# Kernel optimization log

Hardware: AMD Instinct MI355X
Metric: run time of the kernel (lower is better)

## Reference

```python
import jax, jax.numpy as jnp
import numpy as np

EPS = 1e-9
LAM_SEL, LAM_ID, LAM_RATE, LAM_KL, LAM_ENT, LAM_SMOOTH = 1.0, 10.0, 5.0, 0.1, 0.05, 0.5


def setup_inputs() -> dict:
    T, BS, V, K, RIDS = 48, 256, 4096, 32, 1024
    key = jax.random.key(0)
    ks = jax.random.split(key, 10)
    selector_logits = jax.random.normal(ks[0], (BS, 2, K), dtype=jnp.float32)
    selector_probs = jax.nn.softmax(jax.random.normal(ks[1], (BS, 2, K)), axis=-1)
    sel_idx = jax.random.randint(ks[2], (BS, 2), 0, K)
    selector_onehot = jax.nn.one_hot(sel_idx, K, dtype=jnp.float32)
    out_ids = jax.nn.softmax(jax.random.normal(ks[3], (T, BS, V)), axis=-1)
    out_rates = jax.random.uniform(ks[4], (T, BS, 1), dtype=jnp.float32)
    lab_idx = jax.random.randint(ks[5], (T + 2, BS), 0, V)
    trg_labels = jax.nn.one_hot(lab_idx, V, dtype=jnp.float32)
    trg_rates = jax.random.uniform(ks[6], (T + 2, BS, 1), dtype=jnp.float32)
    trg_lengths = jax.random.randint(ks[7], (BS,), 4, T + 2).astype(jnp.int32)
    candi_ids = jax.random.randint(ks[8], (BS, 2, K), 0, RIDS).astype(jnp.int32)
    routes = jax.random.randint(ks[9], (BS, V), 0, RIDS).astype(jnp.int32)
    return {
        'selector_logits': selector_logits, 'selector_probs': selector_probs,
        'selector_onehot': selector_onehot, 'out_ids': out_ids, 'out_rates': out_rates,
        'trg_labels': trg_labels, 'trg_rates': trg_rates, 'trg_lengths': trg_lengths,
        'candi_ids': candi_ids, 'routes': routes,
    }


def _align(lab, T_pred):
    T_lab = lab.shape[0]
    if T_lab >= T_pred + 2:
        return lab[1:-1]
    elif T_lab == T_pred:
        return lab
    else:
        pad = T_pred - T_lab
        return jnp.concatenate([lab, jnp.repeat(lab[-1:], pad, axis=0)], axis=0)


def _loss(selector_logits, selector_probs, selector_onehot, out_ids, out_rates,
          trg_labels, trg_rates, trg_lengths, candi_ids, routes):
    bs, _, K = selector_probs.shape
    # --- selector NLL (use_bce_logits=False path) ---
    sel_mask = (selector_onehot.sum(-1) > 0.5).astype(jnp.float32)      # [bs,2]
    sel_p_true = jnp.maximum((selector_probs * selector_onehot).sum(-1), EPS)
    loss_sel = (-jnp.log(sel_p_true) * sel_mask).sum() / jnp.maximum(sel_mask.sum(), 1.0)

    # --- id NLL over aligned target labels ---
    T_pred = out_ids.shape[0]
    tla = _align(trg_labels, T_pred)                                    # [T,bs,V]
    tra = _align(trg_rates, T_pred)                                     # [T,bs,1]
    step_mask = (tla.sum(-1) > 0.5).astype(jnp.float32)                 # [T,bs]
    p_true = jnp.maximum((out_ids * tla).sum(-1), EPS)
    loss_id = (-jnp.log(p_true) * step_mask).sum() * LAM_ID / jnp.maximum(step_mask.sum(), 1.0)

    # --- rate L1 ---
    denom_rate = jnp.maximum(1, (trg_lengths - 2).sum()).astype(jnp.float32)
    loss_rate = jnp.abs(out_rates - tra).sum() * LAM_RATE / denom_rate

    # --- KL over per-batch candidate unions (vectorized dedup via first-occurrence) ---
    U2 = 2 * K
    ids = candi_ids.reshape(bs, U2)                                     # [bs,2K]
    probs_flat = selector_probs.reshape(bs, U2)                         # [bs,2K]
    eq = ids[:, :, None] == ids[:, None, :]                             # [bs,2K,2K]
    rep = jnp.argmax(eq, axis=-1)                                       # first occurrence idx
    slots = jnp.arange(U2)
    valid = (rep == slots[None, :]).astype(jnp.float32)                 # [bs,2K] union slots
    Ucnt = valid.sum(-1)                                                # [bs]
    # Pm: scatter-add selector probs onto union slots (duplicates summed)
    rep_oh = (rep[:, :, None] == slots[None, None, :]).astype(jnp.float32)  # [bs,2K,2K]
    Pm = jnp.einsum('biu,bi->bu', rep_oh, probs_flat)                   # [bs,2K]
    Pm = Pm / jnp.maximum(Pm.sum(-1, keepdims=True), EPS)
    # Pb: project route mass onto union ids
    dist_r = out_ids.sum(0)                                             # [bs,V]
    match = (routes[:, :, None] == ids[:, None, :]).astype(jnp.float32)  # [bs,V,2K]
    agg = jnp.einsum('bvu,bv->bu', match, dist_r) * valid               # [bs,2K]
    s = agg.sum(-1, keepdims=True)                                      # [bs,1]
    uniform = valid / jnp.maximum(Ucnt, 1.0)[:, None]
    Pb = jnp.where(s > 0, agg / jnp.maximum(s, EPS), uniform)
    Pb_c = jnp.maximum(Pb, EPS)
    kl_b = (Pb_c * (jnp.log(Pb_c) - jnp.log(jnp.maximum(Pm, EPS))) * valid).sum(-1)
    loss_kl = LAM_KL * (kl_b.sum() / max(1, bs))

    # --- entropy of selector probs ---
    p = jnp.maximum(selector_probs, EPS)                                # [bs,2,K]
    ent_b = 0.5 * (-(p * jnp.log(p)).sum(-1)).sum(-1)                   # [bs]
    loss_entropy = LAM_ENT * (ent_b.sum() / max(1, bs))

    # --- rate smoothness ---
    r = out_rates[..., 0]                                               # [T,bs]
    dr = jnp.abs(r[1:] - r[:-1])                                        # [T-1,bs]
    eff = jnp.maximum(trg_lengths - 3, 0)                               # [bs]
    smask = (jnp.arange(T_pred - 1)[:, None] < eff[None, :]).astype(jnp.float32)
    loss_smooth = LAM_SMOOTH * (dr * smask).sum()

    return LAM_SEL * loss_sel + loss_id + loss_rate + loss_kl + loss_entropy + loss_smooth


def reference(selector_logits, selector_probs, selector_onehot, out_ids, out_rates,
              trg_labels, trg_rates, trg_lengths, candi_ids, routes):
    return _loss(selector_logits, selector_probs, selector_onehot, out_ids, out_rates,
                 trg_labels, trg_rates, trg_lengths, candi_ids, routes)
```

## Files before the change

kernel.cpp:

```cpp
#include <hip/hip_runtime.h>
#include <math.h>

#define EPSF 1e-9f

typedef float v4f __attribute__((ext_vector_type(4)));


__global__ __launch_bounds__(256) void e2e3_prep(
    const float* __restrict__ selector_probs,
    const int*   __restrict__ candi_ids,
    const int*   __restrict__ routes,
    float* __restrict__ pmlog_g,
    float* __restrict__ valid_g,
    signed char* __restrict__ slot_map,
    float* __restrict__ agg_g,
    float* __restrict__ acc)
{
    const int b   = blockIdx.x;
    const int tid = threadIdx.x;

    __shared__ int   ids_s[64];
    __shared__ int   table[1024];
    __shared__ int   rep_s[64];

    if (tid < 64) agg_g[b * 64 + tid] = 0.f;
    if (b == 0 && tid < 4) acc[tid] = 0.f;

    for (int i = tid; i < 1024; i += 256) table[i] = 64;
    if (tid < 64) ids_s[tid] = candi_ids[b * 64 + tid];
    __syncthreads();
    if (tid < 64) atomicMin(&table[ids_s[tid]], tid);
    __syncthreads();
    if (tid < 64) {
        const int r = table[ids_s[tid]];
        rep_s[tid] = r;
        valid_g[b * 64 + tid] = (r == tid) ? 1.f : 0.f;
    }
    __syncthreads();
    if (tid < 64) {
        float pm = 0.f;
        for (int i = 0; i < 64; ++i)
            if (rep_s[i] == tid) pm += selector_probs[b * 64 + i];
        float tot = pm;
        #pragma unroll
        for (int off = 32; off >= 1; off >>= 1) tot += __shfl_xor(tot, off, 64);
        pm = pm / fmaxf(tot, EPSF);
        pmlog_g[b * 64 + tid] = logf(fmaxf(pm, EPSF));
    }

    const int4* rp = reinterpret_cast<const int4*>(routes + (size_t)b * 4096 + tid * 16);
    signed char smv[16];
    #pragma unroll
    for (int j = 0; j < 4; ++j) {
        const int4 rv = rp[j];
        const int t0 = table[rv.x], t1 = table[rv.y], t2 = table[rv.z], t3 = table[rv.w];
        smv[j * 4 + 0] = (signed char)(t0 < 64 ? t0 : -1);
        smv[j * 4 + 1] = (signed char)(t1 < 64 ? t1 : -1);
        smv[j * 4 + 2] = (signed char)(t2 < 64 ? t2 : -1);
        smv[j * 4 + 3] = (signed char)(t3 < 64 ? t3 : -1);
    }
    *reinterpret_cast<int4*>(slot_map + (size_t)b * 4096 + tid * 16) =
        *reinterpret_cast<const int4*>(smv);
}

__global__ __launch_bounds__(512) void e2e3_stream(
    const float* __restrict__ out_ids,
    const float* __restrict__ trg_labels,
    const signed char* __restrict__ slot_map,
    float* __restrict__ agg_g,
    float* __restrict__ acc)
{
    const int bid  = blockIdx.x;
    const int b    = bid & 255;
    const int g    = bid >> 8;
    const int tid  = threadIdx.x;
    const int wave = tid >> 6;
    const int lane = tid & 63;
    const int v0   = tid << 3;
    const int t0   = g * 12;

    __shared__ float agg_s[64];
    __shared__ float red[2][8];
    if (tid < 64) agg_s[tid] = 0.f;
    __syncthreads();

    const size_t tstride = (size_t)256 * 4096;
    const float* outp = out_ids    + (size_t)t0 * tstride       + (size_t)b * 4096 + v0;
    const float* labp = trg_labels + (size_t)(t0 + 1) * tstride + (size_t)b * 4096 + v0;

    v4f d0 = (v4f)(0.f);
    v4f d1 = (v4f)(0.f);
    float idnum = 0.f, idcnt = 0.f;

    v4f o0 = __builtin_nontemporal_load(reinterpret_cast<const v4f*>(outp));
    v4f o1 = __builtin_nontemporal_load(reinterpret_cast<const v4f*>(outp + 4));
    v4f l0 = __builtin_nontemporal_load(reinterpret_cast<const v4f*>(labp));
    v4f l1 = __builtin_nontemporal_load(reinterpret_cast<const v4f*>(labp + 4));

    for (int t = 0; t < 12; ++t) {
        v4f no0 = o0, no1 = o1, nl0 = l0, nl1 = l1;
        if (t < 11) {
            const size_t off = (size_t)(t + 1) * tstride;
            no0 = __builtin_nontemporal_load(reinterpret_cast<const v4f*>(outp + off));
            no1 = __builtin_nontemporal_load(reinterpret_cast<const v4f*>(outp + off + 4));
            nl0 = __builtin_nontemporal_load(reinterpret_cast<const v4f*>(labp + off));
            nl1 = __builtin_nontemporal_load(reinterpret_cast<const v4f*>(labp + off + 4));
        }
        d0 += o0;
        d1 += o1;
        if (l0.x > 0.5f) { idnum -= logf(fmaxf(o0.x, EPSF)); idcnt += 1.f; }
        if (l0.y > 0.5f) { idnum -= logf(fmaxf(o0.y, EPSF)); idcnt += 1.f; }
        if (l0.z > 0.5f) { idnum -= logf(fmaxf(o0.z, EPSF)); idcnt += 1.f; }
        if (l0.w > 0.5f) { idnum -= logf(fmaxf(o0.w, EPSF)); idcnt += 1.f; }
        if (l1.x > 0.5f) { idnum -= logf(fmaxf(o1.x, EPSF)); idcnt += 1.f; }
        if (l1.y > 0.5f) { idnum -= logf(fmaxf(o1.y, EPSF)); idcnt += 1.f; }
        if (l1.z > 0.5f) { idnum -= logf(fmaxf(o1.z, EPSF)); idcnt += 1.f; }
        if (l1.w > 0.5f) { idnum -= logf(fmaxf(o1.w, EPSF)); idcnt += 1.f; }
        o0 = no0; o1 = no1; l0 = nl0; l1 = nl1;
    }

    {
        const uint2 sv = *reinterpret_cast<const uint2*>(slot_map + (size_t)b * 4096 + v0);
        const unsigned int w0 = sv.x, w1 = sv.y;
        const float dv[8] = {d0.x, d0.y, d0.z, d0.w, d1.x, d1.y, d1.z, d1.w};
        #pragma unroll
        for (int j = 0; j < 4; ++j) {
            const int u0 = (int)(signed char)((w0 >> (8 * j)) & 0xFF);
            if (u0 >= 0) atomicAdd(&agg_s[u0], dv[j]);
            const int u1 = (int)(signed char)((w1 >> (8 * j)) & 0xFF);
            if (u1 >= 0) atomicAdd(&agg_s[u1], dv[4 + j]);
        }
    }

    #pragma unroll
    for (int off = 32; off >= 1; off >>= 1) {
        idnum += __shfl_down(idnum, off, 64);
        idcnt += __shfl_down(idcnt, off, 64);
    }
    if (lane == 0) { red[0][wave] = idnum; red[1][wave] = idcnt; }
    __syncthreads();
    if (tid == 0) {
        float a = 0.f, c = 0.f;
        #pragma unroll
        for (int w = 0; w < 8; ++w) { a += red[0][w]; c += red[1][w]; }
        atomicAdd(&acc[0], a);
        atomicAdd(&acc[1], c);
    }
    if (tid < 64) atomicAdd(&agg_g[b * 64 + tid], agg_s[tid]);
}

__global__ __launch_bounds__(64) void e2e3_kl2(
    const float* __restrict__ agg_g,
    const float* __restrict__ pmlog_g,
    const float* __restrict__ valid_g,
    float* __restrict__ acc)
{
    const int b = blockIdx.x;
    const int u = threadIdx.x;

    const float va = valid_g[b * 64 + u];
    const float a  = (va > 0.5f) ? agg_g[b * 64 + u] : 0.f;
    float s = a, uc = va;
    #pragma unroll
    for (int off = 32; off >= 1; off >>= 1) {
        s  += __shfl_xor(s,  off, 64);
        uc += __shfl_xor(uc, off, 64);
    }
    const float pb = (s > 0.f) ? (a / fmaxf(s, EPSF)) : (va / fmaxf(uc, 1.f));
    float term = 0.f;
    if (va > 0.5f) {
        const float pbc = fmaxf(pb, EPSF);
        term = pbc * (logf(pbc) - pmlog_g[b * 64 + u]);
    }
    #pragma unroll
    for (int off = 32; off >= 1; off >>= 1) term += __shfl_down(term, off, 64);
    if (u == 0) atomicAdd(&acc[2], term);
}

__global__ __launch_bounds__(256) void e2e3_small(
    const float* __restrict__ selector_probs,
    const float* __restrict__ selector_onehot,
    const float* __restrict__ out_rates,
    const float* __restrict__ trg_rates,
    const int*   __restrict__ trg_lengths,
    const float* __restrict__ acc,
    float* __restrict__ out)
{
    const int tid  = threadIdx.x;
    const int wave = tid >> 6;
    const int lane = tid & 63;

    float v_selnum = 0.f, v_selcnt = 0.f, v_ent = 0.f;
    float v_rate = 0.f, v_den = 0.f, v_smooth = 0.f;

    for (int g = tid; g < 512; g += 256) {
        const float* pp = selector_probs  + g * 32;
        const float* oo = selector_onehot + g * 32;
        float p = 0.f, m = 0.f;
        #pragma unroll
        for (int k = 0; k < 32; ++k) { p += pp[k] * oo[k]; m += oo[k]; }
        if (m > 0.5f) { v_selnum += -logf(fmaxf(p, EPSF)); v_selcnt += 1.f; }
    }
    for (int i = tid; i < 256 * 64; i += 256) {
        const float p = fmaxf(selector_probs[i], EPSF);
        v_ent += -p * logf(p);
    }
    for (int i = tid; i < 48 * 256; i += 256)
        v_rate += fabsf(out_rates[i] - trg_rates[i + 256]);
    for (int b2 = tid; b2 < 256; b2 += 256)
        v_den += (float)(trg_lengths[b2] - 2);
    for (int i = tid; i < 47 * 256; i += 256) {
        const int b2 = i & 255;
        const int t  = i >> 8;
        int eff = trg_lengths[b2] - 3; if (eff < 0) eff = 0;
        if (t < eff) v_smooth += fabsf(out_rates[i + 256] - out_rates[i]);
    }

    __shared__ float red[6][4];
    float vals[6] = {v_selnum, v_selcnt, v_ent, v_rate, v_den, v_smooth};
    #pragma unroll
    for (int k = 0; k < 6; ++k) {
        float v = vals[k];
        #pragma unroll
        for (int off = 32; off >= 1; off >>= 1) v += __shfl_down(v, off, 64);
        if (lane == 0) red[k][wave] = v;
    }
    __syncthreads();
    if (tid == 0) {
        float s[6];
        #pragma unroll
        for (int k = 0; k < 6; ++k) s[k] = red[k][0] + red[k][1] + red[k][2] + red[k][3];
        const float loss =
              s[0] / fmaxf(s[1], 1.f)
            + 10.f * acc[0] / fmaxf(acc[1], 1.f)
            + 5.f  * s[3]   / fmaxf(s[4], 1.f)
            + 0.1f * acc[2] * (1.f / 256.f)
            + 0.05f * 0.5f * s[2] * (1.f / 256.f)
            + 0.5f * s[5];
        out[0] = loss;
    }
}

extern "C" void kernel_launch(void* const* d_in, const int* in_sizes, int n_in,
                              void* d_out, int out_size, void* d_ws, size_t ws_size,
                              hipStream_t stream) {
    const float* selector_probs  = (const float*)d_in[1];
    const float* selector_onehot = (const float*)d_in[2];
    const float* out_ids         = (const float*)d_in[3];
    const float* out_rates       = (const float*)d_in[4];
    const float* trg_labels      = (const float*)d_in[5];
    const float* trg_rates       = (const float*)d_in[6];
    const int*   trg_lengths     = (const int*)d_in[7];
    const int*   candi_ids       = (const int*)d_in[8];
    const int*   routes          = (const int*)d_in[9];

    char* ws = (char*)d_ws;
    float*       acc      = (float*)ws;
    float*       agg_g    = (float*)(ws + 256);
    float*       pmlog_g  = (float*)(ws + 256 + 65536);
    float*       valid_g  = (float*)(ws + 256 + 131072);
    signed char* slot_map = (signed char*)(ws + 196864);

    e2e3_prep<<<256, 256, 0, stream>>>(selector_probs, candi_ids, routes,
                                       pmlog_g, valid_g, slot_map,
                                       agg_g, acc);
    e2e3_stream<<<1024, 512, 0, stream>>>(out_ids, trg_labels, slot_map,
                                          agg_g, acc);
    e2e3_kl2<<<256, 64, 0, stream>>>(agg_g, pmlog_g, valid_g, acc);
    e2e3_small<<<1, 256, 0, stream>>>(selector_probs, selector_onehot,
                                      out_rates, trg_rates, trg_lengths,
                                      acc, (float*)d_out);
}
```

Measured before the change: 118.1 us.

## Remap stream kernel to per-thread float4 over strided timesteps with deeper prefetch

Each block now covers half a batch row's vocabulary, with every thread owning 4 contiguous elements. Threads walk 24 timesteps at stride two (timestep parity comes from the block index) instead of 8 elements over 12 timesteps. Loads use a two-deep register prefetch, and out_ids reads switch from nontemporal to normal loads. The slot map is read once up front. The aim is more memory requests in flight and fewer shared atomics per thread, at the cost of longer per-thread loops and reliance on the unchanged grid size for correct indexing.

```diff
diff --git a/kernel.cpp b/kernel.cpp
--- a/kernel.cpp
+++ b/kernel.cpp
@@ -71,66 +71,57 @@
     float* __restrict__ acc)
 {
     const int bid  = blockIdx.x;
-    const int b    = bid & 255;
-    const int g    = bid >> 8;
     const int tid  = threadIdx.x;
     const int wave = tid >> 6;
     const int lane = tid & 63;
-    const int v0   = tid << 3;
-    const int t0   = g * 12;
+
+    const int b = (bid >> 1) & 255;
+    const int v = (bid & 1) * 2048 + tid * 4;
 
     __shared__ float agg_s[64];
     __shared__ float red[2][8];
     if (tid < 64) agg_s[tid] = 0.f;
     __syncthreads();
 
-    const size_t tstride = (size_t)256 * 4096;
-    const float* outp = out_ids    + (size_t)t0 * tstride       + (size_t)b * 4096 + v0;
-    const float* labp = trg_labels + (size_t)(t0 + 1) * tstride + (size_t)b * 4096 + v0;
-
-    v4f d0 = (v4f)(0.f);
-    v4f d1 = (v4f)(0.f);
+    const unsigned int sm =
+        *reinterpret_cast<const unsigned int*>(slot_map + (size_t)b * 4096 + v);
+    const int u0 = (int)(signed char)(sm & 0xFF);
+    const int u1 = (int)(signed char)((sm >> 8) & 0xFF);
+    const int u2 = (int)(signed char)((sm >> 16) & 0xFF);
+    const int u3 = (int)(signed char)((sm >> 24) & 0xFF);
+
+    const size_t STEP = (size_t)2097152;
+    const size_t e0   = (size_t)(bid * 512 + tid) * 4;
+    const float* op = out_ids + e0;
+    const float* lp = trg_labels + e0 + 1048576;
+
+    float s0 = 0.f, s1 = 0.f, s2 = 0.f, s3 = 0.f;
     float idnum = 0.f, idcnt = 0.f;
 
-    v4f o0 = __builtin_nontemporal_load(reinterpret_cast<const v4f*>(outp));
-    v4f o1 = __builtin_nontemporal_load(reinterpret_cast<const v4f*>(outp + 4));
-    v4f l0 = __builtin_nontemporal_load(reinterpret_cast<const v4f*>(labp));
-    v4f l1 = __builtin_nontemporal_load(reinterpret_cast<const v4f*>(labp + 4));
-
-    for (int t = 0; t < 12; ++t) {
-        v4f no0 = o0, no1 = o1, nl0 = l0, nl1 = l1;
-        if (t < 11) {
-            const size_t off = (size_t)(t + 1) * tstride;
-            no0 = __builtin_nontemporal_load(reinterpret_cast<const v4f*>(outp + off));
-            no1 = __builtin_nontemporal_load(reinterpret_cast<const v4f*>(outp + off + 4));
-            nl0 = __builtin_nontemporal_load(reinterpret_cast<const v4f*>(labp + off));
-            nl1 = __builtin_nontemporal_load(reinterpret_cast<const v4f*>(labp + off + 4));
+    v4f oa = *reinterpret_cast<const v4f*>(op);
+    v4f la = __builtin_nontemporal_load(reinterpret_cast<const v4f*>(lp));
+    v4f ob = *reinterpret_cast<const v4f*>(op + STEP);
+    v4f lb = __builtin_nontemporal_load(reinterpret_cast<const v4f*>(lp + STEP));
+
+    for (int s = 0; s < 24; ++s) {
+        v4f oc = (v4f)(0.f), lc = (v4f)(0.f);
+        if (s < 22) {
+            oc = *reinterpret_cast<const v4f*>(op + (size_t)(s + 2) * STEP);
+            lc = __builtin_nontemporal_load(
+                     reinterpret_cast<const v4f*>(lp + (size_t)(s + 2) * STEP));
         }
-        d0 += o0;
-        d1 += o1;
-        if (l0.x > 0.5f) { idnum -= logf(fmaxf(o0.x, EPSF)); idcnt += 1.f; }
-        if (l0.y > 0.5f) { idnum -= logf(fmaxf(o0.y, EPSF)); idcnt += 1.f; }
-        if (l0.z > 0.5f) { idnum -= logf(fmaxf(o0.z, EPSF)); idcnt += 1.f; }
-        if (l0.w > 0.5f) { idnum -= logf(fmaxf(o0.w, EPSF)); idcnt += 1.f; }
-        if (l1.x > 0.5f) { idnum -= logf(fmaxf(o1.x, EPSF)); idcnt += 1.f; }
-        if (l1.y > 0.5f) { idnum -= logf(fmaxf(o1.y, EPSF)); idcnt += 1.f; }
-        if (l1.z > 0.5f) { idnum -= logf(fmaxf(o1.z, EPSF)); idcnt += 1.f; }
-        if (l1.w > 0.5f) { idnum -= logf(fmaxf(o1.w, EPSF)); idcnt += 1.f; }
-        o0 = no0; o1 = no1; l0 = nl0; l1 = nl1;
-    }
-
-    {
-        const uint2 sv = *reinterpret_cast<const uint2*>(slot_map + (size_t)b * 4096 + v0);
-        const unsigned int w0 = sv.x, w1 = sv.y;
-        const float dv[8] = {d0.x, d0.y, d0.z, d0.w, d1.x, d1.y, d1.z, d1.w};
-        #pragma unroll
-        for (int j = 0; j < 4; ++j) {
-            const int u0 = (int)(signed char)((w0 >> (8 * j)) & 0xFF);
-            if (u0 >= 0) atomicAdd(&agg_s[u0], dv[j]);
-            const int u1 = (int)(signed char)((w1 >> (8 * j)) & 0xFF);
-            if (u1 >= 0) atomicAdd(&agg_s[u1], dv[4 + j]);
-        }
-    }
+        s0 += oa.x; s1 += oa.y; s2 += oa.z; s3 += oa.w;
+        if (la.x > 0.5f) { idnum -= logf(fmaxf(oa.x, EPSF)); idcnt += 1.f; }
+        if (la.y > 0.5f) { idnum -= logf(fmaxf(oa.y, EPSF)); idcnt += 1.f; }
+        if (la.z > 0.5f) { idnum -= logf(fmaxf(oa.z, EPSF)); idcnt += 1.f; }
+        if (la.w > 0.5f) { idnum -= logf(fmaxf(oa.w, EPSF)); idcnt += 1.f; }
+        oa = ob; la = lb; ob = oc; lb = lc;
+    }
+
+    if (u0 >= 0) atomicAdd(&agg_s[u0], s0);
+    if (u1 >= 0) atomicAdd(&agg_s[u1], s1);
+    if (u2 >= 0) atomicAdd(&agg_s[u2], s2);
+    if (u3 >= 0) atomicAdd(&agg_s[u3], s3);
 
     #pragma unroll
     for (int off = 32; off >= 1; off >>= 1) {
```

After: 116.3 us. About the same (-1.5%).
